# Kernel tuning notes

Hardware: AMD Instinct MI355X
Metric: run time of the kernel (lower is better)

Reference implementation:

```python
import jax, jax.numpy as jnp
import numpy as np

B, C, H, W = 4, 256, 64, 64
D, K = 256, 32
EPS = 1e-12  # F.normalize clamp

def setup_inputs() -> dict:
    key = jax.random.key(0)
    k1, k2, k3, k4 = jax.random.split(key, 4)
    x = jax.random.normal(k1, (B, C, H, W), dtype=jnp.float32)
    w_theta = jax.random.normal(k2, (D, C), dtype=jnp.float32) * 0.05  # 1x1 conv theta
    w_phi = jax.random.normal(k3, (K, C // K), dtype=jnp.float32) * 0.1  # grouped 1x1 conv phi
    scale = jax.random.uniform(k4, (D, K), dtype=jnp.float32, minval=-1.0, maxval=0.0)
    return {"x": x, "w_theta": w_theta, "w_phi": w_phi, "scale": scale}

def reference(x, w_theta, w_phi, scale):
    b, c, h, w = x.shape
    d, k = scale.shape
    n = h * w
    xf = x.reshape(b, c, n)                                   # B,D,N (C==D)
    # --- Gen_code ---
    xg = xf.reshape(b, k, c // k, n)                          # grouped 1x1 conv
    x_phi = jnp.einsum('bkcn,kc->bnk', xg, w_phi)             # B,N,K
    x_phi = jax.nn.softmax(x_phi, axis=1)                     # softmax over pixels
    x_theta = jnp.einsum('dc,bcn->bdn', w_theta, xf)          # B,D,N
    code = jnp.einsum('bdn,bnk->bdk', x_theta, x_phi)         # B,D,K
    code = code / jnp.maximum(jnp.linalg.norm(code, axis=1, keepdims=True), EPS)
    # (dropout p=0.15 treated as identity)
    # --- embedded residual, without materializing B,N,D,K ---
    s2 = scale * scale                                        # D,K
    t1 = jnp.einsum('bdn,dk->bnk', xf * xf, s2)
    t2 = jnp.einsum('bdn,bdk->bnk', xf, s2[None] * code)
    t3 = jnp.einsum('dk,bdk->bk', s2, code * code)
    dist = t1 - 2.0 * t2 + t3[:, None, :]                     # sum_d (scale*(x-code))^2
    Q = jax.nn.softmax(-0.5 * dist, axis=2)                   # B,N,K
    Qsum = Q.sum(axis=1)                                      # B,K
    # Z_[b,d,k] = sum_n Q*residual / Qsum = scale*(sum_n Q x / Qsum - code)
    Z_ = scale[None] * (jnp.einsum('bdn,bnk->bdk', xf, Q) / Qsum[:, None, :] - code)
    Z = Z_ / jnp.sqrt((Z_ * Z_).sum(axis=1, keepdims=True))   # torch sqrt, no eps
    return Z, Q
```

## Files before the change

kernel.cpp:

```cpp
#include <hip/hip_runtime.h>
#include <math.h>

#define BB 4
#define CC 256
#define NN 4096
#define KK 32
#define DD 256
#define GG 8
#define NT2 64
#define NE 8
#define NSL 64

__device__ __forceinline__ float wredsum(float v) {
#pragma unroll
  for (int o = 32; o > 0; o >>= 1) v += __shfl_xor(v, o, 64);
  return v;
}

__global__ __launch_bounds__(256) void k_pm1(const float* __restrict__ x,
                                             const float* __restrict__ wphi,
                                             float* __restrict__ m1e,
                                             float* __restrict__ SpE) {
  const int b = blockIdx.x >> 8;
  const int ct = (blockIdx.x >> 6) & 3;
  const int e = blockIdx.x & 63;
  const int n0 = e * 64;
  const int tid = threadIdx.x;
  __shared__ float phis[64 * 33];
  {
    const int kk = tid >> 3;
    const int m = tid & 7;
    const float* xb = x + (size_t)(b * CC + kk * GG) * NN + n0 + m * 8;
    float w[GG];
#pragma unroll
    for (int j = 0; j < GG; ++j) w[j] = wphi[kk * GG + j];
    float4 s0 = make_float4(0.f, 0.f, 0.f, 0.f);
    float4 s1 = make_float4(0.f, 0.f, 0.f, 0.f);
#pragma unroll
    for (int j = 0; j < GG; ++j) {
      const float4 xa = *reinterpret_cast<const float4*>(xb + (size_t)j * NN);
      const float4 xc = *reinterpret_cast<const float4*>(xb + (size_t)j * NN + 4);
      s0.x = fmaf(xa.x, w[j], s0.x);
      s0.y = fmaf(xa.y, w[j], s0.y);
      s0.z = fmaf(xa.z, w[j], s0.z);
      s0.w = fmaf(xa.w, w[j], s0.w);
      s1.x = fmaf(xc.x, w[j], s1.x);
      s1.y = fmaf(xc.y, w[j], s1.y);
      s1.z = fmaf(xc.z, w[j], s1.z);
      s1.w = fmaf(xc.w, w[j], s1.w);
    }
    const int nb = m * 8;
    phis[(nb + 0) * 33 + kk] = __expf(s0.x);
    phis[(nb + 1) * 33 + kk] = __expf(s0.y);
    phis[(nb + 2) * 33 + kk] = __expf(s0.z);
    phis[(nb + 3) * 33 + kk] = __expf(s0.w);
    phis[(nb + 4) * 33 + kk] = __expf(s1.x);
    phis[(nb + 5) * 33 + kk] = __expf(s1.y);
    phis[(nb + 6) * 33 + kk] = __expf(s1.z);
    phis[(nb + 7) * 33 + kk] = __expf(s1.w);
  }
  __syncthreads();
  if (ct == 0 && tid < 32) {
    float s = 0.f;
#pragma unroll 8
    for (int n = 0; n < 64; ++n) s += phis[n * 33 + tid];
    SpE[((size_t)e * BB + b) * KK + tid] = s;
  }
  const int k = tid & 31;
  const int g = tid >> 5;
  const int c0 = ct * 64 + g * 8;
  const float* xm = x + (size_t)(b * CC + c0) * NN + n0;
  float acc[8] = {0.f, 0.f, 0.f, 0.f, 0.f, 0.f, 0.f, 0.f};
  for (int n = 0; n < 64; n += 4) {
    const float p0 = phis[(n + 0) * 33 + k];
    const float p1 = phis[(n + 1) * 33 + k];
    const float p2 = phis[(n + 2) * 33 + k];
    const float p3 = phis[(n + 3) * 33 + k];
#pragma unroll
    for (int c = 0; c < 8; ++c) {
      const float4 xv = *reinterpret_cast<const float4*>(xm + (size_t)c * NN + n);
      acc[c] = fmaf(xv.x, p0, acc[c]);
      acc[c] = fmaf(xv.y, p1, acc[c]);
      acc[c] = fmaf(xv.z, p2, acc[c]);
      acc[c] = fmaf(xv.w, p3, acc[c]);
    }
  }
  float* mb = m1e + (((size_t)e * BB + b) * KK + k) * CC + c0;
  float4 o0 = make_float4(acc[0], acc[1], acc[2], acc[3]);
  float4 o1 = make_float4(acc[4], acc[5], acc[6], acc[7]);
  *reinterpret_cast<float4*>(mb + 0) = o0;
  *reinterpret_cast<float4*>(mb + 4) = o1;
}

__global__ __launch_bounds__(256) void k_code(const float* __restrict__ m1e,
                                              const float* __restrict__ SpE,
                                              const float* __restrict__ wth,
                                              const float* __restrict__ scale,
                                              float* __restrict__ code,
                                              float* __restrict__ bc2,
                                              float* __restrict__ s2g,
                                              float* __restrict__ t3) {
  const int b = blockIdx.x >> 5;
  const int k = blockIdx.x & 31;
  const int d = threadIdx.x;
  __shared__ __align__(16) float m1s[CC];
  __shared__ float rb[4];
  float sp = (d < NSL) ? SpE[((size_t)d * BB + b) * KK + k] : 0.f;
  sp = wredsum(sp);
  if ((d & 63) == 0) rb[d >> 6] = sp;
  __syncthreads();
  const float invS = 1.f / (rb[0] + rb[1] + rb[2] + rb[3]);
  float m = 0.f;
  for (int e = 0; e < NSL; ++e)
    m += m1e[(((size_t)e * BB + b) * KK + k) * CC + d];
  m1s[d] = m * invS;
  __syncthreads();
  float c0 = 0.f, c1 = 0.f, c2 = 0.f, c3 = 0.f;
  const float* wt = wth + (size_t)d * CC;
#pragma unroll 4
  for (int c = 0; c < CC; c += 4) {
    const float4 w4 = *reinterpret_cast<const float4*>(wt + c);
    const float4 m4 = *reinterpret_cast<const float4*>(&m1s[c]);
    c0 = fmaf(w4.x, m4.x, c0);
    c1 = fmaf(w4.y, m4.y, c1);
    c2 = fmaf(w4.z, m4.z, c2);
    c3 = fmaf(w4.w, m4.w, c3);
  }
  float cd = (c0 + c1) + (c2 + c3);
  float ss = wredsum(cd * cd);
  __syncthreads();
  if ((d & 63) == 0) rb[d >> 6] = ss;
  __syncthreads();
  const float nrm = sqrtf(rb[0] + rb[1] + rb[2] + rb[3]);
  const float inv = 1.f / fmaxf(nrm, 1e-12f);
  cd *= inv;
  const float sc = scale[(size_t)d * KK + k];
  const float s2 = sc * sc;
  code[((size_t)b * DD + d) * KK + k] = cd;
  bc2[((size_t)b * DD + d) * KK + k] = 2.f * s2 * cd;
  if (b == 0) s2g[(size_t)d * KK + k] = s2;
  float tt = wredsum(s2 * cd * cd);
  __syncthreads();
  if ((d & 63) == 0) rb[d >> 6] = tt;
  __syncthreads();
  if (d == 0) t3[b * KK + k] = rb[0] + rb[1] + rb[2] + rb[3];
}

__global__ __launch_bounds__(1024) void k_dist(const float* __restrict__ x,
                                               const float* __restrict__ s2g,
                                               const float* __restrict__ bc2,
                                               const float* __restrict__ t3,
                                               float* __restrict__ qout,
                                               float* __restrict__ qpart) {
  const int b = blockIdx.x >> 6;
  const int tile = blockIdx.x & 63;
  const int n0 = tile * 64;
  const int tid = threadIdx.x;
  const int lane = tid & 63;
  const int wid = __builtin_amdgcn_readfirstlane(tid >> 6);
  const int d0 = wid * 16;
  __shared__ float lds[4 * 64 * 33];
  __shared__ float smax[64 * 9];
  __shared__ float ssum[64 * 9];
  float accA[32], accB[32];
#pragma unroll
  for (int k = 0; k < 32; ++k) { accA[k] = 0.f; accB[k] = 0.f; }
  const float* xb = x + ((size_t)b * CC + d0) * NN + n0 + lane;
  const float* s2b = s2g + (size_t)d0 * KK;
  const float* bcb = bc2 + ((size_t)b * DD + d0) * KK;
#pragma unroll 2
  for (int dd = 0; dd < 16; ++dd) {
    const float xv = xb[(size_t)dd * NN];
    const float x2 = xv * xv;
    const float* s2r = s2b + dd * KK;
    const float* bcr = bcb + dd * KK;
#pragma unroll
    for (int k = 0; k < 32; ++k) {
      accA[k] = fmaf(x2, s2r[k], accA[k]);
      accB[k] = fmaf(xv, bcr[k], accB[k]);
    }
  }
  if (wid >= 12) {
    float* Lp = lds + ((size_t)((wid - 12) * 64 + lane)) * 33;
#pragma unroll
    for (int k = 0; k < 32; ++k) Lp[k] = accA[k] - accB[k];
  }
  __syncthreads();
  if (wid >= 8 && wid < 12) {
    float* Lp = lds + ((size_t)((wid - 8) * 64 + lane)) * 33;
#pragma unroll
    for (int k = 0; k < 32; ++k) Lp[k] += accA[k] - accB[k];
  }
  __syncthreads();
  if (wid >= 4 && wid < 8) {
    float* Lp = lds + ((size_t)((wid - 4) * 64 + lane)) * 33;
#pragma unroll
    for (int k = 0; k < 32; ++k) Lp[k] += accA[k] - accB[k];
  }
  __syncthreads();
  if (wid < 4) {
    float* Lp = lds + ((size_t)(wid * 64 + lane)) * 33;
#pragma unroll
    for (int k = 0; k < 32; ++k) Lp[k] += accA[k] - accB[k];
  }
  __syncthreads();
  const int n = lane;
  const int kq = wid;
  float vals[4];
  float e[4];
  if (wid < 8) {
#pragma unroll
    for (int j = 0; j < 4; ++j) {
      const int k = kq * 4 + j;
      float s = 0.f;
#pragma unroll
      for (int g = 0; g < 4; ++g) s += lds[((size_t)(g * 64 + n)) * 33 + k];
      vals[j] = -0.5f * (s + t3[b * KK + k]);
    }
    float m4 = fmaxf(fmaxf(vals[0], vals[1]), fmaxf(vals[2], vals[3]));
    smax[n * 9 + kq] = m4;
  }
  __syncthreads();
  if (wid < 8) {
    float m = smax[n * 9 + 0];
#pragma unroll
    for (int g = 1; g < 8; ++g) m = fmaxf(m, smax[n * 9 + g]);
    float ps = 0.f;
#pragma unroll
    for (int j = 0; j < 4; ++j) {
      e[j] = __expf(vals[j] - m);
      ps += e[j];
    }
    ssum[n * 9 + kq] = ps;
  }
  __syncthreads();
  if (wid < 8) {
    float tot = 0.f;
#pragma unroll
    for (int g = 0; g < 8; ++g) tot += ssum[n * 9 + g];
    const float inv = 1.f / tot;
    float4 q4;
    q4.x = e[0] * inv; q4.y = e[1] * inv;
    q4.z = e[2] * inv; q4.w = e[3] * inv;
    *reinterpret_cast<float4*>(qout + ((size_t)b * NN + n0 + n) * KK + kq * 4) =
        q4;
    float qs[4] = {q4.x, q4.y, q4.z, q4.w};
#pragma unroll
    for (int j = 0; j < 4; ++j) {
      const float v = wredsum(qs[j]);
      if (n == 0) qpart[((size_t)b * KK + kq * 4 + j) * NT2 + tile] = v;
    }
  }
}

__global__ __launch_bounds__(256) void k_xp(const float* __restrict__ x,
                                            const float* __restrict__ p,
                                            float* __restrict__ outq) {
  const int e = blockIdx.x & 7;
  const int ct = (blockIdx.x >> 3) & 31;
  const int b = blockIdx.x >> 8;
  const int tid = threadIdx.x;
  const int k = tid & 31;
  const int g = tid >> 5;
  const int n0 = e * 512 + g * 64;
  const float* xb = x + (size_t)(b * CC + ct * 8) * NN;
  const float* pb = p + (size_t)b * NN * KK + k;
  float acc[8] = {0.f, 0.f, 0.f, 0.f, 0.f, 0.f, 0.f, 0.f};
  for (int n = n0; n < n0 + 64; n += 4) {
    const float p0 = pb[(size_t)(n + 0) * KK];
    const float p1 = pb[(size_t)(n + 1) * KK];
    const float p2 = pb[(size_t)(n + 2) * KK];
    const float p3 = pb[(size_t)(n + 3) * KK];
#pragma unroll
    for (int c = 0; c < 8; ++c) {
      const float4 xv = *reinterpret_cast<const float4*>(xb + (size_t)c * NN + n);
      acc[c] = fmaf(xv.x, p0, acc[c]);
      acc[c] = fmaf(xv.y, p1, acc[c]);
      acc[c] = fmaf(xv.z, p2, acc[c]);
      acc[c] = fmaf(xv.w, p3, acc[c]);
    }
  }
  __shared__ float lds[8 * 8 * 33];
#pragma unroll
  for (int c = 0; c < 8; ++c) lds[(g * 8 + c) * 33 + k] = acc[c];
  __syncthreads();
  const int c2 = tid & 7, k2 = tid >> 3;
  float s = 0.f;
#pragma unroll
  for (int gg = 0; gg < 8; ++gg) s += lds[(gg * 8 + c2) * 33 + k2];
  outq[((size_t)(e * BB + b) * KK + k2) * CC + ct * 8 + c2] = s;
}

__global__ __launch_bounds__(256) void k_z(const float* __restrict__ znq8,
                                           const float* __restrict__ code,
                                           const float* __restrict__ scale,
                                           const float* __restrict__ qpart,
                                           float* __restrict__ zout) {
  const int b = blockIdx.x >> 5;
  const int k = blockIdx.x & 31;
  const int d = threadIdx.x;
  __shared__ float rb[4];
  float qp = (d < NT2) ? qpart[((size_t)b * KK + k) * NT2 + d] : 0.f;
  qp = wredsum(qp);
  if ((d & 63) == 0) rb[d >> 6] = qp;
  __syncthreads();
  const float qs = rb[0] + rb[1] + rb[2] + rb[3];
  float zn = 0.f;
#pragma unroll
  for (int e = 0; e < NE; ++e)
    zn += znq8[((size_t)(e * BB + b) * KK + k) * CC + d];
  const float cd = code[((size_t)b * DD + d) * KK + k];
  const float z_ = scale[(size_t)d * KK + k] * (zn / qs - cd);
  float ss = wredsum(z_ * z_);
  __syncthreads();
  if ((d & 63) == 0) rb[d >> 6] = ss;
  __syncthreads();
  const float rn = 1.f / sqrtf(rb[0] + rb[1] + rb[2] + rb[3]);
  zout[((size_t)b * DD + d) * KK + k] = z_ * rn;
}

extern "C" void kernel_launch(void* const* d_in, const int* in_sizes, int n_in,
                              void* d_out, int out_size, void* d_ws,
                              size_t ws_size, hipStream_t stream) {
  const float* x = (const float*)d_in[0];
  const float* wth = (const float*)d_in[1];
  const float* wphi = (const float*)d_in[2];
  const float* scale = (const float*)d_in[3];
  float* out = (float*)d_out;
  float* zout = out;
  float* qout = out + (size_t)BB * DD * KK;
  float* ws = (float*)d_ws;
  float* SpE = ws;
  float* m1e = SpE + (size_t)NSL * BB * KK;
  float* code = m1e + (size_t)NSL * BB * KK * CC;
  float* bc2 = code + (size_t)BB * DD * KK;
  float* s2g = bc2 + (size_t)BB * DD * KK;
  float* t3 = s2g + (size_t)DD * KK;
  float* qpart = t3 + BB * KK;
  float* znq8 = qpart + (size_t)BB * KK * NT2;

  k_pm1<<<BB * NSL * 4, 256, 0, stream>>>(x, wphi, m1e, SpE);
  k_code<<<BB * KK, 256, 0, stream>>>(m1e, SpE, wth, scale, code, bc2, s2g, t3);
  k_dist<<<BB * NT2, 1024, 0, stream>>>(x, s2g, bc2, t3, qout, qpart);
  k_xp<<<BB * 32 * NE, 256, 0, stream>>>(x, qout, znq8);
  k_z<<<BB * KK, 256, 0, stream>>>(znq8, code, scale, qpart, zout);
}
```

Baseline: 72.68 us.

## Fuse x·Q accumulation into dist kernel and reduce per-tile partials in k_z

```diff
diff --git a/kernel.cpp b/kernel.cpp
--- a/kernel.cpp
+++ b/kernel.cpp
@@ -8,7 +8,6 @@
 #define DD 256
 #define GG 8
 #define NT2 64
-#define NE 8
 #define NSL 64
 
 __device__ __forceinline__ float wredsum(float v) {
@@ -111,6 +110,7 @@
   __syncthreads();
   const float invS = 1.f / (rb[0] + rb[1] + rb[2] + rb[3]);
   float m = 0.f;
+#pragma unroll 8
   for (int e = 0; e < NSL; ++e)
     m += m1e[(((size_t)e * BB + b) * KK + k) * CC + d];
   m1s[d] = m * invS;
@@ -151,7 +151,8 @@
                                                const float* __restrict__ bc2,
                                                const float* __restrict__ t3,
                                                float* __restrict__ qout,
-                                               float* __restrict__ qpart) {
+                                               float* __restrict__ qpart,
+                                               float* __restrict__ znt) {
   const int b = blockIdx.x >> 6;
   const int tile = blockIdx.x & 63;
   const int n0 = tile * 64;
@@ -162,22 +163,25 @@
   __shared__ float lds[4 * 64 * 33];
   __shared__ float smax[64 * 9];
   __shared__ float ssum[64 * 9];
+  __shared__ float qlds[64 * 33];
   float accA[32], accB[32];
 #pragma unroll
   for (int k = 0; k < 32; ++k) { accA[k] = 0.f; accB[k] = 0.f; }
-  const float* xb = x + ((size_t)b * CC + d0) * NN + n0 + lane;
-  const float* s2b = s2g + (size_t)d0 * KK;
-  const float* bcb = bc2 + ((size_t)b * DD + d0) * KK;
+  {
+    const float* xb = x + ((size_t)b * CC + d0) * NN + n0 + lane;
+    const float* s2b = s2g + (size_t)d0 * KK;
+    const float* bcb = bc2 + ((size_t)b * DD + d0) * KK;
 #pragma unroll 2
-  for (int dd = 0; dd < 16; ++dd) {
-    const float xv = xb[(size_t)dd * NN];
-    const float x2 = xv * xv;
-    const float* s2r = s2b + dd * KK;
-    const float* bcr = bcb + dd * KK;
-#pragma unroll
-    for (int k = 0; k < 32; ++k) {
-      accA[k] = fmaf(x2, s2r[k], accA[k]);
-      accB[k] = fmaf(xv, bcr[k], accB[k]);
+    for (int dd = 0; dd < 16; ++dd) {
+      const float xv = xb[(size_t)dd * NN];
+      const float x2 = xv * xv;
+      const float* s2r = s2b + dd * KK;
+      const float* bcr = bcb + dd * KK;
+#pragma unroll
+      for (int k = 0; k < 32; ++k) {
+        accA[k] = fmaf(x2, s2r[k], accA[k]);
+        accB[k] = fmaf(xv, bcr[k], accB[k]);
+      }
     }
   }
   if (wid >= 12) {
@@ -244,6 +248,8 @@
     q4.z = e[2] * inv; q4.w = e[3] * inv;
     *reinterpret_cast<float4*>(qout + ((size_t)b * NN + n0 + n) * KK + kq * 4) =
         q4;
+    float* qr = qlds + n * 33 + kq * 4;
+    qr[0] = q4.x; qr[1] = q4.y; qr[2] = q4.z; qr[3] = q4.w;
     float qs[4] = {q4.x, q4.y, q4.z, q4.w};
 #pragma unroll
     for (int j = 0; j < 4; ++j) {
@@ -251,47 +257,45 @@
       if (n == 0) qpart[((size_t)b * KK + kq * 4 + j) * NT2 + tile] = v;
     }
   }
-}
-
-__global__ __launch_bounds__(256) void k_xp(const float* __restrict__ x,
-                                            const float* __restrict__ p,
-                                            float* __restrict__ outq) {
-  const int e = blockIdx.x & 7;
-  const int ct = (blockIdx.x >> 3) & 31;
-  const int b = blockIdx.x >> 8;
-  const int tid = threadIdx.x;
-  const int k = tid & 31;
-  const int g = tid >> 5;
-  const int n0 = e * 512 + g * 64;
-  const float* xb = x + (size_t)(b * CC + ct * 8) * NN;
-  const float* pb = p + (size_t)b * NN * KK + k;
-  float acc[8] = {0.f, 0.f, 0.f, 0.f, 0.f, 0.f, 0.f, 0.f};
-  for (int n = n0; n < n0 + 64; n += 4) {
-    const float p0 = pb[(size_t)(n + 0) * KK];
-    const float p1 = pb[(size_t)(n + 1) * KK];
-    const float p2 = pb[(size_t)(n + 2) * KK];
-    const float p3 = pb[(size_t)(n + 3) * KK];
-#pragma unroll
-    for (int c = 0; c < 8; ++c) {
-      const float4 xv = *reinterpret_cast<const float4*>(xb + (size_t)c * NN + n);
-      acc[c] = fmaf(xv.x, p0, acc[c]);
-      acc[c] = fmaf(xv.y, p1, acc[c]);
-      acc[c] = fmaf(xv.z, p2, acc[c]);
-      acc[c] = fmaf(xv.w, p3, acc[c]);
-    }
-  }
-  __shared__ float lds[8 * 8 * 33];
-#pragma unroll
-  for (int c = 0; c < 8; ++c) lds[(g * 8 + c) * 33 + k] = acc[c];
-  __syncthreads();
-  const int c2 = tid & 7, k2 = tid >> 3;
-  float s = 0.f;
-#pragma unroll
-  for (int gg = 0; gg < 8; ++gg) s += lds[(gg * 8 + c2) * 33 + k2];
-  outq[((size_t)(e * BB + b) * KK + k2) * CC + ct * 8 + c2] = s;
-}
-
-__global__ __launch_bounds__(256) void k_z(const float* __restrict__ znq8,
+  __syncthreads();
+  {
+    const int k3 = tid & 31;
+    const int cg = tid >> 5;
+    const int c0 = cg * 8;
+    float acc[8];
+#pragma unroll
+    for (int c = 0; c < 8; ++c) acc[c] = 0.f;
+    const float* xq = x + ((size_t)b * CC + c0) * NN + n0;
+    for (int nn = 0; nn < 64; nn += 4) {
+      const float q0 = qlds[(nn + 0) * 33 + k3];
+      const float q1 = qlds[(nn + 1) * 33 + k3];
+      const float q2 = qlds[(nn + 2) * 33 + k3];
+      const float q3 = qlds[(nn + 3) * 33 + k3];
+#pragma unroll
+      for (int c = 0; c < 8; ++c) {
+        const float4 xv =
+            *reinterpret_cast<const float4*>(xq + (size_t)c * NN + nn);
+        acc[c] = fmaf(xv.x, q0, acc[c]);
+        acc[c] = fmaf(xv.y, q1, acc[c]);
+        acc[c] = fmaf(xv.z, q2, acc[c]);
+        acc[c] = fmaf(xv.w, q3, acc[c]);
+      }
+    }
+#pragma unroll
+    for (int c = 0; c < 8; ++c) lds[(c0 + c) * 33 + k3] = acc[c];
+    __syncthreads();
+    const int k2 = tid >> 5;
+    const int c2 = (tid & 31) * 8;
+    float v[8];
+#pragma unroll
+    for (int j = 0; j < 8; ++j) v[j] = lds[(c2 + j) * 33 + k2];
+    float* zb = znt + (((size_t)(b * NT2 + tile)) * KK + k2) * CC + c2;
+    *reinterpret_cast<float4*>(zb + 0) = make_float4(v[0], v[1], v[2], v[3]);
+    *reinterpret_cast<float4*>(zb + 4) = make_float4(v[4], v[5], v[6], v[7]);
+  }
+}
+
+__global__ __launch_bounds__(256) void k_z(const float* __restrict__ znt,
                                            const float* __restrict__ code,
                                            const float* __restrict__ scale,
                                            const float* __restrict__ qpart,
@@ -305,10 +309,17 @@
   if ((d & 63) == 0) rb[d >> 6] = qp;
   __syncthreads();
   const float qs = rb[0] + rb[1] + rb[2] + rb[3];
-  float zn = 0.f;
-#pragma unroll
-  for (int e = 0; e < NE; ++e)
-    zn += znq8[((size_t)(e * BB + b) * KK + k) * CC + d];
+  const float* zp = znt + ((size_t)(b * NT2) * KK + k) * CC + d;
+  const size_t tstr = (size_t)KK * CC;
+  float z0 = 0.f, z1 = 0.f, z2 = 0.f, z3 = 0.f;
+#pragma unroll 4
+  for (int t = 0; t < NT2; t += 4) {
+    z0 += zp[(size_t)(t + 0) * tstr];
+    z1 += zp[(size_t)(t + 1) * tstr];
+    z2 += zp[(size_t)(t + 2) * tstr];
+    z3 += zp[(size_t)(t + 3) * tstr];
+  }
+  const float zn = (z0 + z1) + (z2 + z3);
   const float cd = code[((size_t)b * DD + d) * KK + k];
   const float z_ = scale[(size_t)d * KK + k] * (zn / qs - cd);
   float ss = wredsum(z_ * z_);
@@ -337,11 +348,10 @@
   float* s2g = bc2 + (size_t)BB * DD * KK;
   float* t3 = s2g + (size_t)DD * KK;
   float* qpart = t3 + BB * KK;
-  float* znq8 = qpart + (size_t)BB * KK * NT2;
+  float* znt = qpart + (size_t)BB * KK * NT2;
 
   k_pm1<<<BB * NSL * 4, 256, 0, stream>>>(x, wphi, m1e, SpE);
   k_code<<<BB * KK, 256, 0, stream>>>(m1e, SpE, wth, scale, code, bc2, s2g, t3);
-  k_dist<<<BB * NT2, 1024, 0, stream>>>(x, s2g, bc2, t3, qout, qpart);
-  k_xp<<<BB * 32 * NE, 256, 0, stream>>>(x, qout, znq8);
-  k_z<<<BB * KK, 256, 0, stream>>>(znq8, code, scale, qpart, zout);
-}
+  k_dist<<<BB * NT2, 1024, 0, stream>>>(x, s2g, bc2, t3, qout, qpart, znt);
+  k_z<<<BB * KK, 256, 0, stream>>>(znt, code, scale, qpart, zout);
+}
```

Result: slower. 79.55 us (+9.5%).
